# Performance work log

Hardware: AMD Instinct MI355X
Metric: run time of the kernel (lower is better)

The kernel has to match this reference:

```python
import jax, jax.numpy as jnp
import numpy as np

B = 65536
R = 160            # radial_len (capped at MAX_RADIAL_LEN)
EDGE_SINK_WIDTH = 8


def setup_inputs() -> dict:
    key = jax.random.key(0)
    k1, k2 = jax.random.split(key)
    return {
        "history": jax.random.uniform(k1, (B, R, 3), dtype=jnp.float32),
        "color_rgb": jax.random.uniform(k2, (B, 3), dtype=jnp.float32),
        "offset_per_frame_60hz": jnp.float32(1.3),
        "persistence_per_frame_60hz": jnp.float32(0.92),
        "diffusion01": jnp.float32(0.5),
        "dt_seconds": jnp.float32(1.0 / 60.0),
        "amount01": jnp.float32(0.8),
        "spread01": jnp.float32(0.4),
    }


def _forward(history, color_rgb, offset, persistence, diffusion01, dt_seconds, amount01, spread01):
    dt = jnp.clip(dt_seconds, 0.0, 0.05)
    dt_scale = dt * 60.0
    dt_offset = offset * dt_scale
    dt_persist = persistence ** dt_scale

    # ---- inject at centre: 5-bin spread kernel, then clamp to [0,1] ----
    amount = jnp.clip(amount01, 0.0, 1.0)
    spread = jnp.clip(spread01, 0.0, 1.0)
    energy = color_rgb * amount                      # [B,3]
    tight = 1.0 - spread
    w = jnp.stack([0.5 + 0.4 * tight,
                   0.2 * spread + 0.05,
                   0.12 * spread,
                   0.06 * spread,
                   0.02 * spread])                   # [5]
    h = history.at[:, :5, :].add(energy[:, None, :] * w[None, :, None])
    h = jnp.clip(h, 0.0, 1.0)

    # ---- semi-Lagrangian push advection (vectorized scatter-add) ----
    i = jnp.arange(R, dtype=h.dtype)                 # source bin positions
    new_pos = i + dt_offset
    valid = (new_pos >= 0.0) & (new_pos < R - 1)     # bins outside are dropped
    left = jnp.clip(jnp.floor(new_pos).astype(jnp.int32), 0, R - 2)
    frac = new_pos - left.astype(h.dtype)
    wl = jnp.where(valid, (1.0 - frac) * dt_persist, 0.0)  # [R]
    wr = jnp.where(valid, frac * dt_persist, 0.0)
    work = jnp.zeros_like(h)
    work = work.at[:, left, :].add(h * wl[None, :, None])
    work = work.at[:, left + 1, :].add(h * wr[None, :, None])
    h = work

    # ---- diffusion: [k, 1-2k, k] stencil with ZERO boundary taps ----
    k = 0.15 * diffusion01
    c = 1.0 - 2.0 * k
    padded = jnp.pad(h, ((0, 0), (1, 1), (0, 0)))    # zero pad matches torch boundary
    h = c * h + k * padded[:, :-2, :] + k * padded[:, 2:, :]

    # ---- quadratic edge sink over last EDGE_SINK_WIDTH bins ----
    idx = jnp.arange(R)
    t = (R - 1 - idx).astype(h.dtype) / float(EDGE_SINK_WIDTH)
    fade = jnp.where(idx >= R - EDGE_SINK_WIDTH, t * t, jnp.ones((), h.dtype))
    h = h * fade[None, :, None]
    return h


def reference(history, color_rgb, offset_per_frame_60hz, persistence_per_frame_60hz,
              diffusion01, dt_seconds, amount01, spread01):
    return _forward(history, color_rgb, offset_per_frame_60hz,
                    persistence_per_frame_60hz, diffusion01, dt_seconds,
                    amount01, spread01)
```

## Files before the change

kernel.cpp:

```cpp
#include <hip/hip_runtime.h>
#include <math.h>

#define RBINS 160
#define BROWS 65536
#define ROWELEMS 480
#define NELEM (BROWS * ROWELEMS)
#define COLS 40
#define ITER 4
#define NSLOTS (BROWS / ITER)
#define NTHREADS 256
#define NBLOCKS (NSLOTS * COLS / NTHREADS)

__device__ __forceinline__ float clamp01(float x) {
    return __builtin_amdgcn_fmed3f(x, 0.0f, 1.0f);
}

template<int P>
__device__ __forceinline__ void process_rows(
    const float* __restrict__ hist, const float* __restrict__ color,
    float* __restrict__ out, int slot, int a0, int e0,
    const float* gp , const float* aw , bool need_inject)
{
    float G[24];
    #pragma unroll
    for (int q = 0; q < 24; ++q) G[q] = gp[q];

    const float4* src = (const float4*)hist;
    for (int it = 0; it < ITER; ++it) {
        const int b = it * NSLOTS + slot;
        const int base = b * ROWELEMS;
        float w[32];
        const int f0 = (base + a0) >> 2;
        #pragma unroll
        for (int q = 0; q < 8; ++q) {
            int f = f0 + q;
            f = min(max(f, 0), NELEM / 4 - 1);
            float4 v = src[f];
            w[4*q+0] = v.x; w[4*q+1] = v.y; w[4*q+2] = v.z; w[4*q+3] = v.w;
        }
        if (need_inject) {
            const float c0 = color[b*3+0], c1 = color[b*3+1], c2 = color[b*3+2];
            #pragma unroll
            for (int u = 0; u < 32; ++u) {
                const int e = a0 + u;
                if (e >= 0 && e < 15) {
                    const int i  = e / 3;
                    const int cc = e - 3*i;
                    const float cv = (cc == 0) ? c0 : ((cc == 1) ? c1 : c2);
                    w[u] += cv * aw[i];
                }
            }
        }
        #pragma unroll
        for (int u = 0; u < 32; ++u) w[u] = clamp01(w[u]);

        float r[12];
        #pragma unroll
        for (int m = 0; m < 12; ++m) {
            const int gb = (m / 3) * 6;
            float acc = G[gb+0] * w[P+m];
            acc += G[gb+1] * w[P+m+3];
            acc += G[gb+2] * w[P+m+6];
            acc += G[gb+3] * w[P+m+9];
            acc += G[gb+4] * w[P+m+12];
            acc += G[gb+5] * w[P+m+15];
            r[m] = acc;
        }
        float4* dst = (float4*)(out + base + e0);
        dst[0] = make_float4(r[0], r[1], r[2],  r[3]);
        dst[1] = make_float4(r[4], r[5], r[6],  r[7]);
        dst[2] = make_float4(r[8], r[9], r[10], r[11]);
    }
}

__global__ __launch_bounds__(NTHREADS, 4) void beat_kernel(
    const float* __restrict__ hist,
    const float* __restrict__ color,
    const float* __restrict__ p_offset,
    const float* __restrict__ p_persist,
    const float* __restrict__ p_diff,
    const float* __restrict__ p_dt,
    const float* __restrict__ p_amount,
    const float* __restrict__ p_spread,
    float* __restrict__ out)
{
    __shared__ float g_lds[RBINS * 6];
    __shared__ float aw_lds[8];
    __shared__ int   d_lds;

    const int tid = threadIdx.x;

    if (tid < RBINS) {
        const float offs = *p_offset;
        const float pers = *p_persist;
        const float diff = *p_diff;
        const float dts  = *p_dt;

        const float dt       = fminf(fmaxf(dts, 0.0f), 0.05f);
        const float dt_scale = dt * 60.0f;
        const float s        = offs * dt_scale;
        const float dt_pers  = powf(pers, dt_scale);
        const int   dfl      = (int)floorf(s);
        const float kk = 0.15f * diff;
        const float cc = 1.0f - 2.0f * kk;

        const int j = tid;
        float fade = 1.0f;
        if (j >= RBINS - 8) {
            const float tt = (float)(RBINS - 1 - j) * 0.125f;
            fade = tt * tt;
        }
        const int i0 = j - dfl - 3;
        #pragma unroll
        for (int t = 0; t < 6; ++t) {
            float coef = 0.0f;
            const int i = i0 + t;
            if (i >= 0 && i < RBINS) {
                const float np_ = (float)i + s;
                if (np_ >= 0.0f && np_ < (float)(RBINS - 1)) {
                    int left = (int)floorf(np_);
                    left = min(max(left, 0), RBINS - 2);
                    const float frac = np_ - (float)left;
                    const float wl = (1.0f - frac) * dt_pers;
                    const float wr = frac * dt_pers;
                    const int dl = j - left;
                    const int dr = j - (left + 1);
                    const float cl = (dl == 0) ? cc : ((dl == 1 || dl == -1) ? kk : 0.0f);
                    const float cr = (dr == 0) ? cc : ((dr == 1 || dr == -1) ? kk : 0.0f);
                    coef = wl * cl + wr * cr;
                }
            }
            g_lds[j * 6 + t] = coef * fade;
        }
        if (tid == 0) {
            const float am = fminf(fmaxf(*p_amount, 0.0f), 1.0f);
            const float sp = fminf(fmaxf(*p_spread, 0.0f), 1.0f);
            const float tight = 1.0f - sp;
            aw_lds[0] = am * (0.5f + 0.4f * tight);
            aw_lds[1] = am * (0.2f * sp + 0.05f);
            aw_lds[2] = am * (0.12f * sp);
            aw_lds[3] = am * (0.06f * sp);
            aw_lds[4] = am * (0.02f * sp);
            d_lds = dfl;
        }
    }
    __syncthreads();

    const int gid  = blockIdx.x * NTHREADS + tid;
    const int col  = gid % COLS;
    const int slot = gid / COLS;
    const int e0   = col * 12;
    const int j0   = col * 4;

    const int dfl = d_lds;
    const int S   = (dfl + 3) * 3;
    const int p   = (-S) & 3;
    const int a0  = e0 - S - p;
    const bool need_inject = (a0 < 15) && (a0 + 31 >= 0);

    const float* gp = &g_lds[j0 * 6];
    switch (p) {
        case 0: process_rows<0>(hist, color, out, slot, a0, e0, gp, aw_lds, need_inject); break;
        case 1: process_rows<1>(hist, color, out, slot, a0, e0, gp, aw_lds, need_inject); break;
        case 2: process_rows<2>(hist, color, out, slot, a0, e0, gp, aw_lds, need_inject); break;
        default: process_rows<3>(hist, color, out, slot, a0, e0, gp, aw_lds, need_inject); break;
    }
}

extern "C" void kernel_launch(void* const* d_in, const int* in_sizes, int n_in,
                              void* d_out, int out_size, void* d_ws, size_t ws_size,
                              hipStream_t stream) {
    const float* hist      = (const float*)d_in[0];
    const float* color     = (const float*)d_in[1];
    const float* p_offset  = (const float*)d_in[2];
    const float* p_persist = (const float*)d_in[3];
    const float* p_diff    = (const float*)d_in[4];
    const float* p_dt      = (const float*)d_in[5];
    const float* p_amount  = (const float*)d_in[6];
    const float* p_spread  = (const float*)d_in[7];
    float* outp = (float*)d_out;

    beat_kernel<<<dim3(NBLOCKS), dim3(NTHREADS), 0, stream>>>(
        hist, color, p_offset, p_persist, p_diff, p_dt, p_amount, p_spread, outp);
}
```

Baseline: 247.9 us.

## Stage row tiles in LDS with coalesced loads and inject in shared memory

Each block now copies an 8-row tile of history into LDS with coalesced float4 loads, applies the centre injection directly in LDS, then has each thread read its overlapping 32-element window from LDS. This replaces the redundant overlapping global reads and per-thread inject branching. Each thread now handles one row instead of four, so there are more blocks. That adds per-block coefficient setup and extra barriers, and LDS usage may limit occupancy.

```diff
diff --git a/kernel.cpp b/kernel.cpp
--- a/kernel.cpp
+++ b/kernel.cpp
@@ -5,72 +5,52 @@
 #define BROWS 65536
 #define ROWELEMS 480
 #define NELEM (BROWS * ROWELEMS)
-#define COLS 40
-#define ITER 4
-#define NSLOTS (BROWS / ITER)
-#define NTHREADS 256
-#define NBLOCKS (NSLOTS * COLS / NTHREADS)
+#define TILE_ROWS 8
+#define TILE_F (TILE_ROWS * ROWELEMS)
+#define TILE_F4 (TILE_F / 4)
+#define NTHREADS 320
+#define NBLOCKS (BROWS / TILE_ROWS)
 
 __device__ __forceinline__ float clamp01(float x) {
     return __builtin_amdgcn_fmed3f(x, 0.0f, 1.0f);
 }
 
 template<int P>
-__device__ __forceinline__ void process_rows(
-    const float* __restrict__ hist, const float* __restrict__ color,
-    float* __restrict__ out, int slot, int a0, int e0,
-    const float* gp , const float* aw , bool need_inject)
+__device__ __forceinline__ void compute_store(
+    const float4* __restrict__ tile4, const float* __restrict__ gp,
+    float* __restrict__ outp, int w4base)
 {
+    float w[32];
+    #pragma unroll
+    for (int q = 0; q < 8; ++q) {
+        int idx = w4base + q;
+        idx = min(max(idx, 0), TILE_F4 - 1);
+        float4 v = tile4[idx];
+        w[4*q+0] = v.x; w[4*q+1] = v.y; w[4*q+2] = v.z; w[4*q+3] = v.w;
+    }
+    #pragma unroll
+    for (int u = 0; u < 32; ++u) w[u] = clamp01(w[u]);
+
     float G[24];
     #pragma unroll
     for (int q = 0; q < 24; ++q) G[q] = gp[q];
 
-    const float4* src = (const float4*)hist;
-    for (int it = 0; it < ITER; ++it) {
-        const int b = it * NSLOTS + slot;
-        const int base = b * ROWELEMS;
-        float w[32];
-        const int f0 = (base + a0) >> 2;
-        #pragma unroll
-        for (int q = 0; q < 8; ++q) {
-            int f = f0 + q;
-            f = min(max(f, 0), NELEM / 4 - 1);
-            float4 v = src[f];
-            w[4*q+0] = v.x; w[4*q+1] = v.y; w[4*q+2] = v.z; w[4*q+3] = v.w;
-        }
-        if (need_inject) {
-            const float c0 = color[b*3+0], c1 = color[b*3+1], c2 = color[b*3+2];
-            #pragma unroll
-            for (int u = 0; u < 32; ++u) {
-                const int e = a0 + u;
-                if (e >= 0 && e < 15) {
-                    const int i  = e / 3;
-                    const int cc = e - 3*i;
-                    const float cv = (cc == 0) ? c0 : ((cc == 1) ? c1 : c2);
-                    w[u] += cv * aw[i];
-                }
-            }
-        }
-        #pragma unroll
-        for (int u = 0; u < 32; ++u) w[u] = clamp01(w[u]);
-
-        float r[12];
-        #pragma unroll
-        for (int m = 0; m < 12; ++m) {
-            const int gb = (m / 3) * 6;
-            float acc = G[gb+0] * w[P+m];
-            acc += G[gb+1] * w[P+m+3];
-            acc += G[gb+2] * w[P+m+6];
-            acc += G[gb+3] * w[P+m+9];
-            acc += G[gb+4] * w[P+m+12];
-            acc += G[gb+5] * w[P+m+15];
-            r[m] = acc;
-        }
-        float4* dst = (float4*)(out + base + e0);
-        dst[0] = make_float4(r[0], r[1], r[2],  r[3]);
-        dst[1] = make_float4(r[4], r[5], r[6],  r[7]);
-        dst[2] = make_float4(r[8], r[9], r[10], r[11]);
+    float r[12];
+    #pragma unroll
+    for (int m = 0; m < 12; ++m) {
+        const int gb = (m / 3) * 6;
+        float acc = G[gb+0] * w[P+m+0];
+        acc += G[gb+1] * w[P+m+3];
+        acc += G[gb+2] * w[P+m+6];
+        acc += G[gb+3] * w[P+m+9];
+        acc += G[gb+4] * w[P+m+12];
+        acc += G[gb+5] * w[P+m+15];
+        r[m] = acc;
     }
+    float4* dst = (float4*)outp;
+    dst[0] = make_float4(r[0], r[1], r[2],  r[3]);
+    dst[1] = make_float4(r[4], r[5], r[6],  r[7]);
+    dst[2] = make_float4(r[8], r[9], r[10], r[11]);
 }
 
 __global__ __launch_bounds__(NTHREADS, 4) void beat_kernel(
@@ -84,6 +64,7 @@
     const float* __restrict__ p_spread,
     float* __restrict__ out)
 {
+    __shared__ float tile[TILE_F];
     __shared__ float g_lds[RBINS * 6];
     __shared__ float aw_lds[8];
     __shared__ int   d_lds;
@@ -144,26 +125,49 @@
             d_lds = dfl;
         }
     }
+
+    {
+        const float4* src = (const float4*)hist;
+        float4* t4 = (float4*)tile;
+        const int base4 = blockIdx.x * TILE_F4;
+        #pragma unroll
+        for (int q = 0; q < TILE_F4 / NTHREADS; ++q) {
+            const int idx = q * NTHREADS + tid;
+            t4[idx] = src[base4 + idx];
+        }
+    }
     __syncthreads();
 
-    const int gid  = blockIdx.x * NTHREADS + tid;
-    const int col  = gid % COLS;
-    const int slot = gid / COLS;
-    const int e0   = col * 12;
-    const int j0   = col * 4;
+    if (tid < TILE_ROWS * 15) {
+        const int r = tid / 15;
+        const int e = tid - r * 15;
+        const int i = e / 3;
+        const int ch = e - 3 * i;
+        const int b = blockIdx.x * TILE_ROWS + r;
+        tile[r * ROWELEMS + e] += color[b * 3 + ch] * aw_lds[i];
+    }
+    __syncthreads();
+
+    const int r  = tid / 40;
+    const int c  = tid - r * 40;
+    const int e0 = c * 12;
+    const int j0 = c * 4;
 
     const int dfl = d_lds;
     const int S   = (dfl + 3) * 3;
     const int p   = (-S) & 3;
     const int a0  = e0 - S - p;
-    const bool need_inject = (a0 < 15) && (a0 + 31 >= 0);
+    const int w4base = r * (ROWELEMS / 4) + (a0 >> 2);
 
     const float* gp = &g_lds[j0 * 6];
+    float* outp = out + (blockIdx.x * TILE_ROWS + r) * ROWELEMS + e0;
+    const float4* tile4 = (const float4*)tile;
+
     switch (p) {
-        case 0: process_rows<0>(hist, color, out, slot, a0, e0, gp, aw_lds, need_inject); break;
-        case 1: process_rows<1>(hist, color, out, slot, a0, e0, gp, aw_lds, need_inject); break;
-        case 2: process_rows<2>(hist, color, out, slot, a0, e0, gp, aw_lds, need_inject); break;
-        default: process_rows<3>(hist, color, out, slot, a0, e0, gp, aw_lds, need_inject); break;
+        case 0:  compute_store<0>(tile4, gp, outp, w4base); break;
+        case 1:  compute_store<1>(tile4, gp, outp, w4base); break;
+        case 2:  compute_store<2>(tile4, gp, outp, w4base); break;
+        default: compute_store<3>(tile4, gp, outp, w4base); break;
     }
 }
 
```

Result: faster. 236.7 us (-4.5%).
